# Performance work log

Measured on AMD Instinct MI355X. Metric: run time of the kernel, lower is better.

Reference implementation:

```python
import jax, jax.numpy as jnp
import numpy as np

EPS = 1e-5

def _layernorm(x, gamma, beta):
    # normalize over last (channel) axis, per point
    mu = jnp.mean(x, axis=-1, keepdims=True)
    var = jnp.mean(jnp.square(x - mu), axis=-1, keepdims=True)
    return (x - mu) * jax.lax.rsqrt(var + EPS) * gamma + beta

def setup_inputs() -> dict:
    key = jax.random.key(0)
    ks = jax.random.split(key, 12)
    B, N, C, F = 32, 4096, 3, 1024
    points = jax.random.normal(ks[0], (B, N, C), dtype=jnp.float32)
    mask = jax.random.randint(ks[1], (B, 1, N), 0, 2, dtype=jnp.int32)
    s = 0.05
    return {
        "points": points,
        "mask": mask,
        "w1": jax.random.normal(ks[2], (128, C), dtype=jnp.float32) * s,      # conv1 (no bias)
        "g1": jnp.ones((128,), jnp.float32),                                   # norm1 gamma
        "be1": jnp.zeros((128,), jnp.float32),                                 # norm1 beta
        "w2": jax.random.normal(ks[3], (256, 128), dtype=jnp.float32) * s,     # conv2
        "b2": jax.random.normal(ks[4], (256,), dtype=jnp.float32) * s,
        "w3": jax.random.normal(ks[5], (512, 512), dtype=jnp.float32) * s,     # conv3 (no bias)
        "g2": jnp.ones((512,), jnp.float32),                                   # norm2 gamma
        "be2": jnp.zeros((512,), jnp.float32),                                 # norm2 beta
        "w4": jax.random.normal(ks[6], (F, 512), dtype=jnp.float32) * s,       # conv4
        "b4": jax.random.normal(ks[7], (F,), dtype=jnp.float32) * s,
    }

def reference(points, mask, w1, g1, be1, w2, b2, w3, g2, be2, w4, b4):
    # points: [B, N, C]; mask: [B, 1, N]
    vis = (mask[:, 0, :] != 0).astype(points.dtype)[..., None]  # [B, N, 1]
    # conv1 (1x1, no bias) as point-wise matmul
    h0 = jnp.einsum('bnc,kc->bnk', points, w1)                  # [B, N, 128]
    # masked LayerNorm: LN is per-point over channels, so compute densely and zero invisible points
    h1 = _layernorm(h0, g1, be1) * vis
    h2 = jax.nn.relu(h1)
    h3 = jnp.einsum('bnk,ok->bno', h2, w2) + b2                 # [B, N, 256]
    gmax = jnp.max(h3, axis=1, keepdims=True)                   # [B, 1, 256]
    dist = jnp.concatenate([jnp.broadcast_to(gmax, h3.shape), h3], axis=-1)  # [B, N, 512]
    h4 = jnp.einsum('bno,po->bnp', dist, w3)                    # [B, N, 512]
    h5 = _layernorm(h4, g2, be2) * vis
    h6 = jax.nn.relu(h5)
    h7 = jnp.einsum('bnp,fp->bnf', h6, w4) + b4                 # [B, N, F]
    return jnp.max(h7, axis=1)                                  # [B, F]
```

## Files before the change

kernel.cpp:

```cpp
#include <hip/hip_runtime.h>
#include <stdint.h>

#define LN_EPS 1e-5f

static __device__ __forceinline__ unsigned short f2bf_bits(float f) {
  union { float f; unsigned u; } v; v.f = f;
  unsigned r = v.u + 0x7FFFu + ((v.u >> 16) & 1u);
  return (unsigned short)(r >> 16);
}
static __device__ __forceinline__ float bf2f(unsigned short h) {
  union { unsigned u; float f; } v; v.u = ((unsigned)h) << 16;
  return v.f;
}

typedef __bf16 bf16x8 __attribute__((ext_vector_type(8)));
typedef float floatx4 __attribute__((ext_vector_type(4)));

typedef __attribute__((address_space(1))) unsigned int* gas_ptr;
typedef __attribute__((address_space(3))) unsigned int* las_ptr;
static __device__ __forceinline__ void async_cp16(const void* g, void* l) {
  __builtin_amdgcn_global_load_lds((gas_ptr)g, (las_ptr)l, 16, 0, 0);
}

__global__ __launch_bounds__(256) void perm_kernel(
    const int* __restrict__ mask, int* __restrict__ newrow, int* __restrict__ cnt) {
  const int b = blockIdx.x, t = threadIdx.x;
  const int base = b * 4096 + t * 16;
  int v[16]; int s = 0;
#pragma unroll
  for (int i = 0; i < 16; ++i) { v[i] = (mask[base + i] != 0); s += v[i]; }
  const int lane = t & 63, wv = t >> 6;
  int scan = s;
  for (int o = 1; o < 64; o <<= 1) { int x = __shfl_up(scan, o); if (lane >= o) scan += x; }
  __shared__ int wsum[4], woff[4], stotal;
  if (lane == 63) wsum[wv] = scan;
  __syncthreads();
  if (t == 0) { int a = 0; for (int k = 0; k < 4; ++k) { woff[k] = a; a += wsum[k]; } stotal = a; cnt[b] = a; }
  __syncthreads();
  const int excl = scan - s + woff[wv];
  const int total = stotal;
  int run = 0;
#pragma unroll
  for (int i = 0; i < 16; ++i) {
    const int pos = t * 16 + i;
    const int visBefore = excl + run;
    newrow[b * 4096 + pos] = v[i] ? visBefore : total + (pos - visBefore);
    run += v[i];
  }
}

__global__ __launch_bounds__(256) void conv1_ln_kernel(
    const float* __restrict__ points,
    const float* __restrict__ w1, const float* __restrict__ g1,
    const float* __restrict__ be1, unsigned short* __restrict__ h2,
    const int* __restrict__ newrow, const int* __restrict__ cnt,
    const float* __restrict__ w2, const float* __restrict__ b2,
    const float* __restrict__ w3, const float* __restrict__ w4,
    unsigned short* __restrict__ w2b, unsigned short* __restrict__ w4b,
    unsigned short* __restrict__ w23b, float* __restrict__ vecb) {
  if (blockIdx.x >= 32768) {
    const int bb = blockIdx.x - 32768;
    if (bb < 2176) {
      int idx = bb * 256 + threadIdx.x;
      if (idx < 32768) w2b[idx] = f2bf_bits(w2[idx]);
      else w4b[idx - 32768] = f2bf_bits(w4[idx - 32768]);
    } else {
      const int tid = threadIdx.x;
      const int p = (bb - 2176) * 2 + (tid >> 7);
      const int c = tid & 127;
      const float* w3r = w3 + (size_t)p * 512 + 256;
      float s = 0.f;
      for (int k = 0; k < 256; ++k) s += w3r[k] * w2[k * 128 + c];
      w23b[p * 128 + c] = f2bf_bits(s);
      if (c == 0) {
        float vb = 0.f;
        for (int k = 0; k < 256; ++k) vb += w3r[k] * b2[k];
        vecb[p] = vb;
      }
    }
    return;
  }
  const int lane = threadIdx.x & 63;
  const int wv = threadIdx.x >> 6;
  const size_t p = (size_t)blockIdx.x * 4 + wv;
  const int dest = newrow[p];
  const int cntb = cnt[p >> 12];
  const int ceilv = (cntb + 127) & ~127;
  if (dest >= ceilv) return;
  const bool vis = (dest < cntb);
  const float x0 = points[p * 3 + 0];
  const float x1 = points[p * 3 + 1];
  const float x2 = points[p * 3 + 2];
  const int c0 = lane * 2, c1 = c0 + 1;
  float h00 = w1[c0 * 3] * x0 + w1[c0 * 3 + 1] * x1 + w1[c0 * 3 + 2] * x2;
  float h01 = w1[c1 * 3] * x0 + w1[c1 * 3 + 1] * x1 + w1[c1 * 3 + 2] * x2;
  float s = h00 + h01;
  for (int o = 32; o; o >>= 1) s += __shfl_xor(s, o);
  const float mu = s * (1.f / 128.f);
  const float d0 = h00 - mu, d1 = h01 - mu;
  float q = d0 * d0 + d1 * d1;
  for (int o = 32; o; o >>= 1) q += __shfl_xor(q, o);
  const float rs = rsqrtf(q * (1.f / 128.f) + LN_EPS);
  const float y0 = vis ? fmaxf(d0 * rs * g1[c0] + be1[c0], 0.f) : 0.f;
  const float y1 = vis ? fmaxf(d1 * rs * g1[c1] + be1[c1], 0.f) : 0.f;
  union { unsigned u; unsigned short s2[2]; } pk;
  pk.s2[0] = f2bf_bits(y0);
  pk.s2[1] = f2bf_bits(y1);
  const size_t prow = (p & ~(size_t)4095) + (size_t)dest;
  ((unsigned*)h2)[prow * 64 + lane] = pk.u;
}

__global__ __launch_bounds__(256) void gemm23_fused(
    const unsigned short* __restrict__ A,
    const unsigned short* __restrict__ w2b, const unsigned short* __restrict__ w23b,
    unsigned short* __restrict__ h46, float* __restrict__ pg,
    const float* __restrict__ b2, const float* __restrict__ vecb,
    const int* __restrict__ cnt, int M) {
  __shared__ __align__(16) char smA[2][128 * 64];
  __shared__ __align__(16) char smB[2][128 * 64];
  __shared__ float lmax[2][128];

  const int tid = threadIdx.x;
  const int lane = tid & 63;
  const int w = tid >> 6;
  const int wm = w >> 1, wn = w & 1;

  const int gid = blockIdx.x;
  const int xcd = gid & 7;
  const int slot = gid >> 3;
  const int rowsPerXcd = (M >> 7) >> 3;
  const int rowTile = xcd * rowsPerXcd + slot / 6;
  const int colTile = slot % 6;
  const bool isPG = (colTile < 2);
  const int colBase = isPG ? colTile * 128 : (colTile - 2) * 128;
  const size_t rowBase = (size_t)rowTile * 128;
  const unsigned short* Bw = isPG ? w2b : w23b;

  const int cntb = cnt[rowBase >> 12];
  const int rb = (int)(rowBase & 4095);
  if (rb >= cntb) {
    if (isPG) {
      if (tid < 128) pg[(size_t)rowTile * 256 + colBase + tid] = b2[colBase + tid];
    }
    return;
  }

  floatx4 acc[4][4];
  const floatx4 zero = {0.f, 0.f, 0.f, 0.f};
#pragma unroll
  for (int i = 0; i < 4; ++i)
#pragma unroll
    for (int j = 0; j < 4; ++j) acc[i][j] = zero;

  const int rSub = lane >> 2;
  const int cb16 = (lane & 3) * 16;
  const size_t Kb = 256;
  const char* gA = (const char*)A + (rowBase + (size_t)(w * 32 + rSub)) * Kb + cb16;
  const char* gB = (const char*)Bw + ((size_t)colBase + (size_t)(w * 32 + rSub)) * Kb + cb16;
  char* lA0 = smA[0] + w * 2048;
  char* lA1 = smA[1] + w * 2048;
  char* lB0 = smB[0] + w * 2048;
  char* lB1 = smB[1] + w * 2048;
  const size_t skip16 = 16 * Kb;

  const int fm = lane & 15, fq = lane >> 4;
  const int fOff = fm * 64 + fq * 16;
  const char* pa0 = smA[0] + wm * 64 * 64 + fOff;
  const char* pa1 = smA[1] + wm * 64 * 64 + fOff;
  const char* pb0 = smB[0] + wn * 64 * 64 + fOff;
  const char* pb1 = smB[1] + wn * 64 * 64 + fOff;

  for (int k0 = 0; k0 < 128; k0 += 64) {
    async_cp16(gA, lA0);
    async_cp16(gA + skip16, lA0 + 1024);
    async_cp16(gA + 64, lA1);
    async_cp16(gA + 64 + skip16, lA1 + 1024);
    async_cp16(gB, lB0);
    async_cp16(gB + skip16, lB0 + 1024);
    async_cp16(gB + 64, lB1);
    async_cp16(gB + 64 + skip16, lB1 + 1024);
    gA += 128; gB += 128;
    __syncthreads();
    bf16x8 af0[4], bg0[4], af1[4], bg1[4];
#pragma unroll
    for (int i = 0; i < 4; ++i) af0[i] = *(const bf16x8*)(pa0 + i * 16 * 64);
#pragma unroll
    for (int j = 0; j < 4; ++j) bg0[j] = *(const bf16x8*)(pb0 + j * 16 * 64);
#pragma unroll
    for (int i = 0; i < 4; ++i)
#pragma unroll
      for (int j = 0; j < 4; ++j)
        acc[i][j] = __builtin_amdgcn_mfma_f32_16x16x32_bf16(af0[i], bg0[j], acc[i][j], 0, 0, 0);
#pragma unroll
    for (int i = 0; i < 4; ++i) af1[i] = *(const bf16x8*)(pa1 + i * 16 * 64);
#pragma unroll
    for (int j = 0; j < 4; ++j) bg1[j] = *(const bf16x8*)(pb1 + j * 16 * 64);
#pragma unroll
    for (int i = 0; i < 4; ++i)
#pragma unroll
      for (int j = 0; j < 4; ++j)
        acc[i][j] = __builtin_amdgcn_mfma_f32_16x16x32_bf16(af1[i], bg1[j], acc[i][j], 0, 0, 0);
    __syncthreads();
  }

  if (isPG) {
    float m4[4] = {-1e30f, -1e30f, -1e30f, -1e30f};
#pragma unroll
    for (int j = 0; j < 4; ++j) {
      const float ex = b2[colBase + wn * 64 + j * 16 + fm];
#pragma unroll
      for (int i = 0; i < 4; ++i)
#pragma unroll
        for (int r = 0; r < 4; ++r) m4[j] = fmaxf(m4[j], acc[i][j][r] + ex);
      m4[j] = fmaxf(m4[j], __shfl_xor(m4[j], 16));
      m4[j] = fmaxf(m4[j], __shfl_xor(m4[j], 32));
    }
    const float sel = (fq == 0) ? m4[0] : (fq == 1) ? m4[1] : (fq == 2) ? m4[2] : m4[3];
    lmax[wm][wn * 64 + fq * 16 + fm] = sel;
    __syncthreads();
    if (tid < 128) {
      const float v = fmaxf(lmax[0][tid], lmax[1][tid]);
      pg[(size_t)rowTile * 256 + colBase + tid] = v;
    }
  } else {
#pragma unroll
    for (int j = 0; j < 4; ++j) {
      const int col = colBase + wn * 64 + j * 16 + fm;
      const float ex = vecb[col];
#pragma unroll
      for (int i = 0; i < 4; ++i) {
        const size_t row0 = rowBase + wm * 64 + i * 16 + fq * 4;
#pragma unroll
        for (int r = 0; r < 4; ++r) {
          h46[(row0 + r) * 512 + col] = f2bf_bits(acc[i][j][r] + ex);
        }
      }
    }
  }
}

template <int NCT>
__global__ __launch_bounds__(256) void gemm4_kernel(
    const unsigned short* __restrict__ A, const unsigned short* __restrict__ Bw,
    float* __restrict__ outp2, const int* __restrict__ cnt,
    int M, int N, int K) {
  __shared__ __align__(16) char smA[2][128 * 64];
  __shared__ __align__(16) char smB[2][128 * 64];
  __shared__ float lmax[2][128];

  const int tid = threadIdx.x;
  const int lane = tid & 63;
  const int w = tid >> 6;
  const int wm = w >> 1, wn = w & 1;

  const int gid = blockIdx.x;
  const int xcd = gid & 7;
  const int slot = gid >> 3;
  const int rowsPerXcd = (M >> 7) >> 3;
  const int rowTile = xcd * rowsPerXcd + slot / NCT;
  const int colTile = slot % NCT;
  const size_t rowBase = (size_t)rowTile * 128;
  const int colBase = colTile * 128;

  const int cntb = cnt[rowBase >> 12];
  const int rb = (int)(rowBase & 4095);
  if (rb >= cntb) {
    if (tid < 128) outp2[(size_t)rowTile * N + colBase + tid] = 0.f;
    return;
  }

  floatx4 acc[4][4];
  const floatx4 zero = {0.f, 0.f, 0.f, 0.f};
#pragma unroll
  for (int i = 0; i < 4; ++i)
#pragma unroll
    for (int j = 0; j < 4; ++j) acc[i][j] = zero;

  const int rSub = lane >> 2;
  const int cb16 = (lane & 3) * 16;
  const size_t Kb = (size_t)K * 2;
  const char* gA = (const char*)A + (rowBase + (size_t)(w * 32 + rSub)) * Kb + cb16;
  const char* gB = (const char*)Bw + ((size_t)colBase + (size_t)(w * 32 + rSub)) * Kb + cb16;
  char* lA0 = smA[0] + w * 2048;
  char* lA1 = smA[1] + w * 2048;
  char* lB0 = smB[0] + w * 2048;
  char* lB1 = smB[1] + w * 2048;
  const size_t skip16 = 16 * Kb;

  const int fm = lane & 15, fq = lane >> 4;
  const int fOff = fm * 64 + fq * 16;
  const char* pa0 = smA[0] + wm * 64 * 64 + fOff;
  const char* pa1 = smA[1] + wm * 64 * 64 + fOff;
  const char* pb0 = smB[0] + wn * 64 * 64 + fOff;
  const char* pb1 = smB[1] + wn * 64 * 64 + fOff;

  for (int k0 = 0; k0 < K; k0 += 64) {
    async_cp16(gA, lA0);
    async_cp16(gA + skip16, lA0 + 1024);
    async_cp16(gA + 64, lA1);
    async_cp16(gA + 64 + skip16, lA1 + 1024);
    async_cp16(gB, lB0);
    async_cp16(gB + skip16, lB0 + 1024);
    async_cp16(gB + 64, lB1);
    async_cp16(gB + 64 + skip16, lB1 + 1024);
    gA += 128; gB += 128;
    __syncthreads();
    bf16x8 af0[4], bg0[4], af1[4], bg1[4];
#pragma unroll
    for (int i = 0; i < 4; ++i) af0[i] = *(const bf16x8*)(pa0 + i * 16 * 64);
#pragma unroll
    for (int j = 0; j < 4; ++j) bg0[j] = *(const bf16x8*)(pb0 + j * 16 * 64);
#pragma unroll
    for (int i = 0; i < 4; ++i)
#pragma unroll
      for (int j = 0; j < 4; ++j)
        acc[i][j] = __builtin_amdgcn_mfma_f32_16x16x32_bf16(af0[i], bg0[j], acc[i][j], 0, 0, 0);
#pragma unroll
    for (int i = 0; i < 4; ++i) af1[i] = *(const bf16x8*)(pa1 + i * 16 * 64);
#pragma unroll
    for (int j = 0; j < 4; ++j) bg1[j] = *(const bf16x8*)(pb1 + j * 16 * 64);
#pragma unroll
    for (int i = 0; i < 4; ++i)
#pragma unroll
      for (int j = 0; j < 4; ++j)
        acc[i][j] = __builtin_amdgcn_mfma_f32_16x16x32_bf16(af1[i], bg1[j], acc[i][j], 0, 0, 0);
    __syncthreads();
  }

  float m4[4] = {-1e30f, -1e30f, -1e30f, -1e30f};
#pragma unroll
  for (int j = 0; j < 4; ++j) {
#pragma unroll
    for (int i = 0; i < 4; ++i)
#pragma unroll
      for (int r = 0; r < 4; ++r) m4[j] = fmaxf(m4[j], acc[i][j][r]);
    m4[j] = fmaxf(m4[j], __shfl_xor(m4[j], 16));
    m4[j] = fmaxf(m4[j], __shfl_xor(m4[j], 32));
  }
  const float sel = (fq == 0) ? m4[0] : (fq == 1) ? m4[1] : (fq == 2) ? m4[2] : m4[3];
  lmax[wm][wn * 64 + fq * 16 + fm] = sel;
  __syncthreads();
  if (tid < 128) {
    const float v = fmaxf(lmax[0][tid], lmax[1][tid]);
    outp2[(size_t)rowTile * N + colBase + tid] = v;
  }
}

__global__ __launch_bounds__(256) void gmax_cvec_kernel(
    const float* __restrict__ pg, const float* __restrict__ w3,
    float* __restrict__ cvec) {
  __shared__ float gm[256];
  const int b = blockIdx.x >> 2, quarter = blockIdx.x & 3;
  const int t = threadIdx.x;
  float m = -1e30f;
  for (int s = 0; s < 32; ++s) m = fmaxf(m, pg[((size_t)b * 32 + s) * 256 + t]);
  gm[t] = m;
  __syncthreads();
  const int lane = t & 63, wv = t >> 6;
  const float g0 = gm[lane * 4 + 0];
  const float g1 = gm[lane * 4 + 1];
  const float g2v = gm[lane * 4 + 2];
  const float g3 = gm[lane * 4 + 3];
  for (int pp = 0; pp < 32; ++pp) {
    const int p = quarter * 128 + wv * 32 + pp;
    const float4 wr = *(const float4*)(w3 + (size_t)p * 512 + lane * 4);
    float s = wr.x * g0 + wr.y * g1 + wr.z * g2v + wr.w * g3;
    for (int o = 32; o; o >>= 1) s += __shfl_xor(s, o);
    if (lane == 0) cvec[b * 512 + p] = s;
  }
}

__global__ __launch_bounds__(256) void ln2_kernel(
    unsigned short* __restrict__ h46, const int* __restrict__ cnt,
    const float* __restrict__ cvec,
    const float* __restrict__ g2, const float* __restrict__ be2) {
  const int lane = threadIdx.x & 63;
  const int wv = threadIdx.x >> 6;
  const size_t p = (size_t)blockIdx.x * 4 + wv;
  const int cb = cnt[p >> 12];
  const int pin = (int)(p & 4095);
  const int ceilv = (cb + 127) & ~127;
  if (pin >= ceilv) return;
  unsigned short* row = h46 + p * 512;
  const int c0 = lane * 8;
  if (pin >= cb) {
    const uint4 z = {0, 0, 0, 0};
    *(uint4*)(row + c0) = z;
    return;
  }
  const int b = (int)(p >> 12);
  union { uint4 v; unsigned short s[8]; } in;
  in.v = *(const uint4*)(row + c0);
  float cv[8];
  *(float4*)(cv) = *(const float4*)(cvec + b * 512 + c0);
  *(float4*)(cv + 4) = *(const float4*)(cvec + b * 512 + c0 + 4);
  float f[8];
  float s = 0.f;
#pragma unroll
  for (int k = 0; k < 8; ++k) { f[k] = bf2f(in.s[k]) + cv[k]; s += f[k]; }
  for (int o = 32; o; o >>= 1) s += __shfl_xor(s, o);
  const float mu = s * (1.f / 512.f);
  float q = 0.f;
#pragma unroll
  for (int k = 0; k < 8; ++k) { const float d = f[k] - mu; q += d * d; }
  for (int o = 32; o; o >>= 1) q += __shfl_xor(q, o);
  const float rs = rsqrtf(q * (1.f / 512.f) + LN_EPS);
  union { uint4 v; unsigned short s[8]; } outv;
#pragma unroll
  for (int k = 0; k < 8; ++k) {
    const float y = fmaxf((f[k] - mu) * rs * g2[c0 + k] + be2[c0 + k], 0.f);
    outv.s[k] = f2bf_bits(y);
  }
  *(uint4*)(row + c0) = outv.v;
}

__global__ __launch_bounds__(256) void final_kernel(
    const float* __restrict__ pmax, const float* __restrict__ b4,
    float* __restrict__ out) {
  const int idx = blockIdx.x * 256 + threadIdx.x;
  const int b = idx >> 10, f = idx & 1023;
  float m = -1e30f;
  for (int r = 0; r < 32; ++r) m = fmaxf(m, pmax[((size_t)(b * 32 + r)) * 1024 + f]);
  out[idx] = m + b4[f];
}

extern "C" void kernel_launch(void* const* d_in, const int* in_sizes, int n_in,
                              void* d_out, int out_size, void* d_ws, size_t ws_size,
                              hipStream_t stream) {
  const float* points = (const float*)d_in[0];
  const int* mask = (const int*)d_in[1];
  const float* w1 = (const float*)d_in[2];
  const float* g1 = (const float*)d_in[3];
  const float* be1 = (const float*)d_in[4];
  const float* w2 = (const float*)d_in[5];
  const float* b2 = (const float*)d_in[6];
  const float* w3 = (const float*)d_in[7];
  const float* g2 = (const float*)d_in[8];
  const float* be2 = (const float*)d_in[9];
  const float* w4 = (const float*)d_in[10];
  const float* b4 = (const float*)d_in[11];
  float* out = (float*)d_out;
  char* ws = (char*)d_ws;

  const size_t OFF_H46 = 0;
  const size_t OFF_H2 = 134217728;
  const size_t OFF_W2B = OFF_H2 + 33554432;
  const size_t OFF_W4B = OFF_W2B + 65536;
  const size_t OFF_W23B = OFF_W4B + 1048576;
  const size_t OFF_VECB = OFF_W23B + 131072;
  const size_t OFF_PG = OFF_VECB + 2048;
  const size_t OFF_CVEC = OFF_PG + 1048576;
  const size_t OFF_PMAX = OFF_CVEC + 65536;
  const size_t OFF_CNT = OFF_PMAX + 4194304;
  const size_t OFF_NEWROW = OFF_CNT + 4096;

  unsigned short* h2 = (unsigned short*)(ws + OFF_H2);
  unsigned short* h46 = (unsigned short*)(ws + OFF_H46);
  unsigned short* w2b = (unsigned short*)(ws + OFF_W2B);
  unsigned short* w4b = (unsigned short*)(ws + OFF_W4B);
  unsigned short* w23b = (unsigned short*)(ws + OFF_W23B);
  float* vecb = (float*)(ws + OFF_VECB);
  float* pg = (float*)(ws + OFF_PG);
  float* cvecp = (float*)(ws + OFF_CVEC);
  float* pmaxp = (float*)(ws + OFF_PMAX);
  int* cntp = (int*)(ws + OFF_CNT);
  int* newrow = (int*)(ws + OFF_NEWROW);

  perm_kernel<<<32, 256, 0, stream>>>(mask, newrow, cntp);
  conv1_ln_kernel<<<32768 + 2176 + 256, 256, 0, stream>>>(
      points, w1, g1, be1, h2, newrow, cntp, w2, b2, w3, w4, w2b, w4b, w23b, vecb);
  gemm23_fused<<<6144, 256, 0, stream>>>(h2, w2b, w23b, h46, pg, b2, vecb, cntp, 131072);
  gmax_cvec_kernel<<<128, 256, 0, stream>>>(pg, w3, cvecp);
  ln2_kernel<<<32768, 256, 0, stream>>>(h46, cntp, cvecp, g2, be2);
  gemm4_kernel<8><<<8192, 256, 0, stream>>>(h46, w4b, pmaxp, cntp, 131072, 1024, 512);
  final_kernel<<<128, 256, 0, stream>>>(pmaxp, b4, out);
}
```

Measured before the change: 276.6 us.

## Merge all stages into one cooperative persistent kernel with grid syncs

Replaces the seven separate kernel launches with a single cooperative mega-kernel. It runs a persistent grid sized from occupancy and separates the stages with grid.sync(). The aim is to remove per-launch overhead and the tail gaps between the small and large kernels. In exchange, blocks loop over virtual block IDs with occupancy capped at 3-4 blocks per CU, and tiles tied to the XCD mapping may lose locality. Each grid-wide barrier also has a cost, and the register pressure of the merged code may limit occupancy.

After: 651.0 us. 2.35x slower.

```diff
diff --git a/kernel.cpp b/kernel.cpp
--- a/kernel.cpp
+++ b/kernel.cpp
@@ -1,5 +1,8 @@
 #include <hip/hip_runtime.h>
+#include <hip/hip_cooperative_groups.h>
 #include <stdint.h>
+
+namespace cg = cooperative_groups;
 
 #define LN_EPS 1e-5f
 
@@ -22,406 +25,379 @@
   __builtin_amdgcn_global_load_lds((gas_ptr)g, (las_ptr)l, 16, 0, 0);
 }
 
-__global__ __launch_bounds__(256) void perm_kernel(
-    const int* __restrict__ mask, int* __restrict__ newrow, int* __restrict__ cnt) {
-  const int b = blockIdx.x, t = threadIdx.x;
-  const int base = b * 4096 + t * 16;
-  int v[16]; int s = 0;
-#pragma unroll
-  for (int i = 0; i < 16; ++i) { v[i] = (mask[base + i] != 0); s += v[i]; }
-  const int lane = t & 63, wv = t >> 6;
-  int scan = s;
-  for (int o = 1; o < 64; o <<= 1) { int x = __shfl_up(scan, o); if (lane >= o) scan += x; }
-  __shared__ int wsum[4], woff[4], stotal;
-  if (lane == 63) wsum[wv] = scan;
-  __syncthreads();
-  if (t == 0) { int a = 0; for (int k = 0; k < 4; ++k) { woff[k] = a; a += wsum[k]; } stotal = a; cnt[b] = a; }
-  __syncthreads();
-  const int excl = scan - s + woff[wv];
-  const int total = stotal;
-  int run = 0;
-#pragma unroll
-  for (int i = 0; i < 16; ++i) {
-    const int pos = t * 16 + i;
-    const int visBefore = excl + run;
-    newrow[b * 4096 + pos] = v[i] ? visBefore : total + (pos - visBefore);
-    run += v[i];
-  }
-}
-
-__global__ __launch_bounds__(256) void conv1_ln_kernel(
-    const float* __restrict__ points,
+__global__ __launch_bounds__(256, 3) void mega_kernel(
+    const float* __restrict__ points, const int* __restrict__ mask,
     const float* __restrict__ w1, const float* __restrict__ g1,
-    const float* __restrict__ be1, unsigned short* __restrict__ h2,
-    const int* __restrict__ newrow, const int* __restrict__ cnt,
-    const float* __restrict__ w2, const float* __restrict__ b2,
-    const float* __restrict__ w3, const float* __restrict__ w4,
+    const float* __restrict__ be1, const float* __restrict__ w2,
+    const float* __restrict__ b2, const float* __restrict__ w3,
+    const float* __restrict__ g2, const float* __restrict__ be2,
+    const float* __restrict__ w4, const float* __restrict__ b4,
+    float* __restrict__ out,
+    unsigned short* __restrict__ h2, unsigned short* __restrict__ h46,
     unsigned short* __restrict__ w2b, unsigned short* __restrict__ w4b,
-    unsigned short* __restrict__ w23b, float* __restrict__ vecb) {
-  if (blockIdx.x >= 32768) {
-    const int bb = blockIdx.x - 32768;
-    if (bb < 2176) {
-      int idx = bb * 256 + threadIdx.x;
-      if (idx < 32768) w2b[idx] = f2bf_bits(w2[idx]);
-      else w4b[idx - 32768] = f2bf_bits(w4[idx - 32768]);
-    } else {
-      const int tid = threadIdx.x;
-      const int p = (bb - 2176) * 2 + (tid >> 7);
-      const int c = tid & 127;
-      const float* w3r = w3 + (size_t)p * 512 + 256;
-      float s = 0.f;
-      for (int k = 0; k < 256; ++k) s += w3r[k] * w2[k * 128 + c];
-      w23b[p * 128 + c] = f2bf_bits(s);
-      if (c == 0) {
-        float vb = 0.f;
-        for (int k = 0; k < 256; ++k) vb += w3r[k] * b2[k];
-        vecb[p] = vb;
-      }
-    }
-    return;
-  }
-  const int lane = threadIdx.x & 63;
-  const int wv = threadIdx.x >> 6;
-  const size_t p = (size_t)blockIdx.x * 4 + wv;
-  const int dest = newrow[p];
-  const int cntb = cnt[p >> 12];
-  const int ceilv = (cntb + 127) & ~127;
-  if (dest >= ceilv) return;
-  const bool vis = (dest < cntb);
-  const float x0 = points[p * 3 + 0];
-  const float x1 = points[p * 3 + 1];
-  const float x2 = points[p * 3 + 2];
-  const int c0 = lane * 2, c1 = c0 + 1;
-  float h00 = w1[c0 * 3] * x0 + w1[c0 * 3 + 1] * x1 + w1[c0 * 3 + 2] * x2;
-  float h01 = w1[c1 * 3] * x0 + w1[c1 * 3 + 1] * x1 + w1[c1 * 3 + 2] * x2;
-  float s = h00 + h01;
-  for (int o = 32; o; o >>= 1) s += __shfl_xor(s, o);
-  const float mu = s * (1.f / 128.f);
-  const float d0 = h00 - mu, d1 = h01 - mu;
-  float q = d0 * d0 + d1 * d1;
-  for (int o = 32; o; o >>= 1) q += __shfl_xor(q, o);
-  const float rs = rsqrtf(q * (1.f / 128.f) + LN_EPS);
-  const float y0 = vis ? fmaxf(d0 * rs * g1[c0] + be1[c0], 0.f) : 0.f;
-  const float y1 = vis ? fmaxf(d1 * rs * g1[c1] + be1[c1], 0.f) : 0.f;
-  union { unsigned u; unsigned short s2[2]; } pk;
-  pk.s2[0] = f2bf_bits(y0);
-  pk.s2[1] = f2bf_bits(y1);
-  const size_t prow = (p & ~(size_t)4095) + (size_t)dest;
-  ((unsigned*)h2)[prow * 64 + lane] = pk.u;
-}
-
-__global__ __launch_bounds__(256) void gemm23_fused(
-    const unsigned short* __restrict__ A,
-    const unsigned short* __restrict__ w2b, const unsigned short* __restrict__ w23b,
-    unsigned short* __restrict__ h46, float* __restrict__ pg,
-    const float* __restrict__ b2, const float* __restrict__ vecb,
-    const int* __restrict__ cnt, int M) {
-  __shared__ __align__(16) char smA[2][128 * 64];
-  __shared__ __align__(16) char smB[2][128 * 64];
-  __shared__ float lmax[2][128];
-
+    unsigned short* __restrict__ w23b, float* __restrict__ vecb,
+    float* __restrict__ pg, float* __restrict__ cvec, float* __restrict__ pmax,
+    int* __restrict__ cnt, int* __restrict__ newrow) {
+  cg::grid_group grid = cg::this_grid();
+  __shared__ __align__(16) char SMEM[33792];
   const int tid = threadIdx.x;
   const int lane = tid & 63;
   const int w = tid >> 6;
+
+  for (int b = blockIdx.x; b < 32; b += gridDim.x) {
+    int* wsum = (int*)SMEM;
+    int* woff = ((int*)SMEM) + 4;
+    int* stot = ((int*)SMEM) + 8;
+    const int base = b * 4096 + tid * 16;
+    int v[16]; int s = 0;
+#pragma unroll
+    for (int i = 0; i < 16; ++i) { v[i] = (mask[base + i] != 0); s += v[i]; }
+    int scan = s;
+    for (int o = 1; o < 64; o <<= 1) { int x = __shfl_up(scan, o); if (lane >= o) scan += x; }
+    if (lane == 63) wsum[w] = scan;
+    __syncthreads();
+    if (tid == 0) {
+      int a = 0;
+      for (int k = 0; k < 4; ++k) { woff[k] = a; a += wsum[k]; }
+      stot[0] = a; cnt[b] = a;
+    }
+    __syncthreads();
+    const int excl = scan - s + woff[w];
+    const int total = stot[0];
+    int run = 0;
+#pragma unroll
+    for (int i = 0; i < 16; ++i) {
+      const int pos = tid * 16 + i;
+      const int visBefore = excl + run;
+      newrow[b * 4096 + pos] = v[i] ? visBefore : total + (pos - visBefore);
+      run += v[i];
+    }
+    __syncthreads();
+  }
+  grid.sync();
+
+  for (int vb = blockIdx.x; vb < 35200; vb += gridDim.x) {
+    if (vb >= 32768) {
+      const int bb = vb - 32768;
+      if (bb < 2176) {
+        int idx = bb * 256 + tid;
+        if (idx < 32768) w2b[idx] = f2bf_bits(w2[idx]);
+        else w4b[idx - 32768] = f2bf_bits(w4[idx - 32768]);
+      } else {
+        const int p = (bb - 2176) * 2 + (tid >> 7);
+        const int c = tid & 127;
+        const float* w3r = w3 + (size_t)p * 512 + 256;
+        float s = 0.f;
+        for (int k = 0; k < 256; ++k) s += w3r[k] * w2[k * 128 + c];
+        w23b[p * 128 + c] = f2bf_bits(s);
+        if (c == 0) {
+          float vbv = 0.f;
+          for (int k = 0; k < 256; ++k) vbv += w3r[k] * b2[k];
+          vecb[p] = vbv;
+        }
+      }
+    } else {
+      const size_t p = (size_t)vb * 4 + w;
+      const int dest = newrow[p];
+      const int cntb = cnt[p >> 12];
+      const int ceilv = (cntb + 127) & ~127;
+      if (dest < ceilv) {
+        const bool vis = (dest < cntb);
+        const float x0 = points[p * 3 + 0];
+        const float x1 = points[p * 3 + 1];
+        const float x2 = points[p * 3 + 2];
+        const int c0 = lane * 2, c1 = c0 + 1;
+        float h00 = w1[c0 * 3] * x0 + w1[c0 * 3 + 1] * x1 + w1[c0 * 3 + 2] * x2;
+        float h01 = w1[c1 * 3] * x0 + w1[c1 * 3 + 1] * x1 + w1[c1 * 3 + 2] * x2;
+        float s = h00 + h01;
+        for (int o = 32; o; o >>= 1) s += __shfl_xor(s, o);
+        const float mu = s * (1.f / 128.f);
+        const float d0 = h00 - mu, d1 = h01 - mu;
+        float q = d0 * d0 + d1 * d1;
+        for (int o = 32; o; o >>= 1) q += __shfl_xor(q, o);
+        const float rs = rsqrtf(q * (1.f / 128.f) + LN_EPS);
+        const float y0 = vis ? fmaxf(d0 * rs * g1[c0] + be1[c0], 0.f) : 0.f;
+        const float y1 = vis ? fmaxf(d1 * rs * g1[c1] + be1[c1], 0.f) : 0.f;
+        union { unsigned u; unsigned short s2[2]; } pk;
+        pk.s2[0] = f2bf_bits(y0);
+        pk.s2[1] = f2bf_bits(y1);
+        const size_t prow = (p & ~(size_t)4095) + (size_t)dest;
+        ((unsigned*)h2)[prow * 64 + lane] = pk.u;
+      }
+    }
+  }
+  grid.sync();
+
+  char* smA0 = SMEM;
+  char* smA1 = SMEM + 8192;
+  char* smB0 = SMEM + 16384;
+  char* smB1 = SMEM + 24576;
+  float* lmax = (float*)(SMEM + 32768);
   const int wm = w >> 1, wn = w & 1;
-
-  const int gid = blockIdx.x;
-  const int xcd = gid & 7;
-  const int slot = gid >> 3;
-  const int rowsPerXcd = (M >> 7) >> 3;
-  const int rowTile = xcd * rowsPerXcd + slot / 6;
-  const int colTile = slot % 6;
-  const bool isPG = (colTile < 2);
-  const int colBase = isPG ? colTile * 128 : (colTile - 2) * 128;
-  const size_t rowBase = (size_t)rowTile * 128;
-  const unsigned short* Bw = isPG ? w2b : w23b;
-
-  const int cntb = cnt[rowBase >> 12];
-  const int rb = (int)(rowBase & 4095);
-  if (rb >= cntb) {
-    if (isPG) {
-      if (tid < 128) pg[(size_t)rowTile * 256 + colBase + tid] = b2[colBase + tid];
-    }
-    return;
-  }
-
-  floatx4 acc[4][4];
-  const floatx4 zero = {0.f, 0.f, 0.f, 0.f};
-#pragma unroll
-  for (int i = 0; i < 4; ++i)
-#pragma unroll
-    for (int j = 0; j < 4; ++j) acc[i][j] = zero;
-
+  const int fm = lane & 15, fq = lane >> 4;
   const int rSub = lane >> 2;
   const int cb16 = (lane & 3) * 16;
-  const size_t Kb = 256;
-  const char* gA = (const char*)A + (rowBase + (size_t)(w * 32 + rSub)) * Kb + cb16;
-  const char* gB = (const char*)Bw + ((size_t)colBase + (size_t)(w * 32 + rSub)) * Kb + cb16;
-  char* lA0 = smA[0] + w * 2048;
-  char* lA1 = smA[1] + w * 2048;
-  char* lB0 = smB[0] + w * 2048;
-  char* lB1 = smB[1] + w * 2048;
-  const size_t skip16 = 16 * Kb;
-
-  const int fm = lane & 15, fq = lane >> 4;
   const int fOff = fm * 64 + fq * 16;
-  const char* pa0 = smA[0] + wm * 64 * 64 + fOff;
-  const char* pa1 = smA[1] + wm * 64 * 64 + fOff;
-  const char* pb0 = smB[0] + wn * 64 * 64 + fOff;
-  const char* pb1 = smB[1] + wn * 64 * 64 + fOff;
-
-  for (int k0 = 0; k0 < 128; k0 += 64) {
-    async_cp16(gA, lA0);
-    async_cp16(gA + skip16, lA0 + 1024);
-    async_cp16(gA + 64, lA1);
-    async_cp16(gA + 64 + skip16, lA1 + 1024);
-    async_cp16(gB, lB0);
-    async_cp16(gB + skip16, lB0 + 1024);
-    async_cp16(gB + 64, lB1);
-    async_cp16(gB + 64 + skip16, lB1 + 1024);
-    gA += 128; gB += 128;
+
+  for (int gid = blockIdx.x; gid < 6144; gid += gridDim.x) {
+    const int xcd = gid & 7;
+    const int slot = gid >> 3;
+    const int rowTile = xcd * 128 + slot / 6;
+    const int colTile = slot % 6;
+    const bool isPG = (colTile < 2);
+    const int colBase = isPG ? colTile * 128 : (colTile - 2) * 128;
+    const size_t rowBase = (size_t)rowTile * 128;
+    const unsigned short* Bw = isPG ? w2b : w23b;
+    const int cntb = cnt[rowBase >> 12];
+    const int rb = (int)(rowBase & 4095);
+    if (rb >= cntb) {
+      if (isPG && tid < 128) pg[(size_t)rowTile * 256 + colBase + tid] = b2[colBase + tid];
+      continue;
+    }
+    floatx4 acc[4][4];
+    const floatx4 zero = {0.f, 0.f, 0.f, 0.f};
+#pragma unroll
+    for (int i = 0; i < 4; ++i)
+#pragma unroll
+      for (int j = 0; j < 4; ++j) acc[i][j] = zero;
+
+    const size_t Kb = 256;
+    const char* gA = (const char*)h2 + (rowBase + (size_t)(w * 32 + rSub)) * Kb + cb16;
+    const char* gB = (const char*)Bw + ((size_t)colBase + (size_t)(w * 32 + rSub)) * Kb + cb16;
+    const size_t skip16 = 16 * Kb;
+    char* lA0 = smA0 + w * 2048;
+    char* lA1 = smA1 + w * 2048;
+    char* lB0 = smB0 + w * 2048;
+    char* lB1 = smB1 + w * 2048;
+    const char* pa0 = smA0 + wm * 64 * 64 + fOff;
+    const char* pa1 = smA1 + wm * 64 * 64 + fOff;
+    const char* pb0 = smB0 + wn * 64 * 64 + fOff;
+    const char* pb1 = smB1 + wn * 64 * 64 + fOff;
+
+    for (int k0 = 0; k0 < 128; k0 += 64) {
+      async_cp16(gA, lA0);
+      async_cp16(gA + skip16, lA0 + 1024);
+      async_cp16(gA + 64, lA1);
+      async_cp16(gA + 64 + skip16, lA1 + 1024);
+      async_cp16(gB, lB0);
+      async_cp16(gB + skip16, lB0 + 1024);
+      async_cp16(gB + 64, lB1);
+      async_cp16(gB + 64 + skip16, lB1 + 1024);
+      gA += 128; gB += 128;
+      __syncthreads();
+      bf16x8 af0[4], bg0[4], af1[4], bg1[4];
+#pragma unroll
+      for (int i = 0; i < 4; ++i) af0[i] = *(const bf16x8*)(pa0 + i * 16 * 64);
+#pragma unroll
+      for (int j = 0; j < 4; ++j) bg0[j] = *(const bf16x8*)(pb0 + j * 16 * 64);
+#pragma unroll
+      for (int i = 0; i < 4; ++i)
+#pragma unroll
+        for (int j = 0; j < 4; ++j)
+          acc[i][j] = __builtin_amdgcn_mfma_f32_16x16x32_bf16(af0[i], bg0[j], acc[i][j], 0, 0, 0);
+#pragma unroll
+      for (int i = 0; i < 4; ++i) af1[i] = *(const bf16x8*)(pa1 + i * 16 * 64);
+#pragma unroll
+      for (int j = 0; j < 4; ++j) bg1[j] = *(const bf16x8*)(pb1 + j * 16 * 64);
+#pragma unroll
+      for (int i = 0; i < 4; ++i)
+#pragma unroll
+        for (int j = 0; j < 4; ++j)
+          acc[i][j] = __builtin_amdgcn_mfma_f32_16x16x32_bf16(af1[i], bg1[j], acc[i][j], 0, 0, 0);
+      __syncthreads();
+    }
+
+    if (isPG) {
+      float m4[4] = {-1e30f, -1e30f, -1e30f, -1e30f};
+#pragma unroll
+      for (int j = 0; j < 4; ++j) {
+        const float ex = b2[colBase + wn * 64 + j * 16 + fm];
+#pragma unroll
+        for (int i = 0; i < 4; ++i)
+#pragma unroll
+          for (int r = 0; r < 4; ++r) m4[j] = fmaxf(m4[j], acc[i][j][r] + ex);
+        m4[j] = fmaxf(m4[j], __shfl_xor(m4[j], 16));
+        m4[j] = fmaxf(m4[j], __shfl_xor(m4[j], 32));
+      }
+      const float sel = (fq == 0) ? m4[0] : (fq == 1) ? m4[1] : (fq == 2) ? m4[2] : m4[3];
+      lmax[wm * 128 + wn * 64 + fq * 16 + fm] = sel;
+      __syncthreads();
+      if (tid < 128) {
+        const float v = fmaxf(lmax[tid], lmax[128 + tid]);
+        pg[(size_t)rowTile * 256 + colBase + tid] = v;
+      }
+    } else {
+#pragma unroll
+      for (int j = 0; j < 4; ++j) {
+        const int col = colBase + wn * 64 + j * 16 + fm;
+        const float ex = vecb[col];
+#pragma unroll
+        for (int i = 0; i < 4; ++i) {
+          const size_t row0 = rowBase + wm * 64 + i * 16 + fq * 4;
+#pragma unroll
+          for (int r = 0; r < 4; ++r) {
+            h46[(row0 + r) * 512 + col] = f2bf_bits(acc[i][j][r] + ex);
+          }
+        }
+      }
+    }
+  }
+  grid.sync();
+
+  if (blockIdx.x < 128) {
+    float* gm = (float*)SMEM;
+    const int b = blockIdx.x >> 2, quarter = blockIdx.x & 3;
+    float m = -1e30f;
+    for (int s = 0; s < 32; ++s) m = fmaxf(m, pg[((size_t)b * 32 + s) * 256 + tid]);
+    gm[tid] = m;
     __syncthreads();
-    bf16x8 af0[4], bg0[4], af1[4], bg1[4];
-#pragma unroll
-    for (int i = 0; i < 4; ++i) af0[i] = *(const bf16x8*)(pa0 + i * 16 * 64);
-#pragma unroll
-    for (int j = 0; j < 4; ++j) bg0[j] = *(const bf16x8*)(pb0 + j * 16 * 64);
+    const float g0 = gm[lane * 4 + 0];
+    const float g1v = gm[lane * 4 + 1];
+    const float g2v = gm[lane * 4 + 2];
+    const float g3 = gm[lane * 4 + 3];
+    for (int pp = 0; pp < 32; ++pp) {
+      const int p = quarter * 128 + w * 32 + pp;
+      const float4 wr = *(const float4*)(w3 + (size_t)p * 512 + lane * 4);
+      float s = wr.x * g0 + wr.y * g1v + wr.z * g2v + wr.w * g3;
+      for (int o = 32; o; o >>= 1) s += __shfl_xor(s, o);
+      if (lane == 0) cvec[b * 512 + p] = s;
+    }
+  }
+  grid.sync();
+
+  for (int vb = blockIdx.x; vb < 32768; vb += gridDim.x) {
+    const size_t p = (size_t)vb * 4 + w;
+    const int cb = cnt[p >> 12];
+    const int pin = (int)(p & 4095);
+    const int ceilv = (cb + 127) & ~127;
+    if (pin >= ceilv) continue;
+    unsigned short* row = h46 + p * 512;
+    const int c0 = lane * 8;
+    if (pin >= cb) {
+      const uint4 z = {0, 0, 0, 0};
+      *(uint4*)(row + c0) = z;
+      continue;
+    }
+    const int b = (int)(p >> 12);
+    union { uint4 v; unsigned short s[8]; } in;
+    in.v = *(const uint4*)(row + c0);
+    float cv[8];
+    *(float4*)(cv) = *(const float4*)(cvec + b * 512 + c0);
+    *(float4*)(cv + 4) = *(const float4*)(cvec + b * 512 + c0 + 4);
+    float f[8];
+    float s = 0.f;
+#pragma unroll
+    for (int k = 0; k < 8; ++k) { f[k] = bf2f(in.s[k]) + cv[k]; s += f[k]; }
+    for (int o = 32; o; o >>= 1) s += __shfl_xor(s, o);
+    const float mu = s * (1.f / 512.f);
+    float q = 0.f;
+#pragma unroll
+    for (int k = 0; k < 8; ++k) { const float d = f[k] - mu; q += d * d; }
+    for (int o = 32; o; o >>= 1) q += __shfl_xor(q, o);
+    const float rs = rsqrtf(q * (1.f / 512.f) + LN_EPS);
+    union { uint4 v; unsigned short s[8]; } outv;
+#pragma unroll
+    for (int k = 0; k < 8; ++k) {
+      const float y = fmaxf((f[k] - mu) * rs * g2[c0 + k] + be2[c0 + k], 0.f);
+      outv.s[k] = f2bf_bits(y);
+    }
+    *(uint4*)(row + c0) = outv.v;
+  }
+  grid.sync();
+
+  for (int gid = blockIdx.x; gid < 8192; gid += gridDim.x) {
+    const int xcd = gid & 7;
+    const int slot = gid >> 3;
+    const int rowTile = xcd * 128 + slot / 8;
+    const int colTile = slot % 8;
+    const size_t rowBase = (size_t)rowTile * 128;
+    const int colBase = colTile * 128;
+    const int cntb = cnt[rowBase >> 12];
+    const int rb = (int)(rowBase & 4095);
+    if (rb >= cntb) {
+      if (tid < 128) pmax[(size_t)rowTile * 1024 + colBase + tid] = 0.f;
+      continue;
+    }
+    floatx4 acc[4][4];
+    const floatx4 zero = {0.f, 0.f, 0.f, 0.f};
 #pragma unroll
     for (int i = 0; i < 4; ++i)
 #pragma unroll
-      for (int j = 0; j < 4; ++j)
-        acc[i][j] = __builtin_amdgcn_mfma_f32_16x16x32_bf16(af0[i], bg0[j], acc[i][j], 0, 0, 0);
-#pragma unroll
-    for (int i = 0; i < 4; ++i) af1[i] = *(const bf16x8*)(pa1 + i * 16 * 64);
-#pragma unroll
-    for (int j = 0; j < 4; ++j) bg1[j] = *(const bf16x8*)(pb1 + j * 16 * 64);
-#pragma unroll
-    for (int i = 0; i < 4; ++i)
-#pragma unroll
-      for (int j = 0; j < 4; ++j)
-        acc[i][j] = __builtin_amdgcn_mfma_f32_16x16x32_bf16(af1[i], bg1[j], acc[i][j], 0, 0, 0);
-    __syncthreads();
-  }
-
-  if (isPG) {
+      for (int j = 0; j < 4; ++j) acc[i][j] = zero;
+
+    const size_t Kb = 1024;
+    const char* gA = (const char*)h46 + (rowBase + (size_t)(w * 32 + rSub)) * Kb + cb16;
+    const char* gB = (const char*)w4b + ((size_t)colBase + (size_t)(w * 32 + rSub)) * Kb + cb16;
+    const size_t skip16 = 16 * Kb;
+    char* lA0 = smA0 + w * 2048;
+    char* lA1 = smA1 + w * 2048;
+    char* lB0 = smB0 + w * 2048;
+    char* lB1 = smB1 + w * 2048;
+    const char* pa0 = smA0 + wm * 64 * 64 + fOff;
+    const char* pa1 = smA1 + wm * 64 * 64 + fOff;
+    const char* pb0 = smB0 + wn * 64 * 64 + fOff;
+    const char* pb1 = smB1 + wn * 64 * 64 + fOff;
+
+    for (int k0 = 0; k0 < 512; k0 += 64) {
+      async_cp16(gA, lA0);
+      async_cp16(gA + skip16, lA0 + 1024);
+      async_cp16(gA + 64, lA1);
+      async_cp16(gA + 64 + skip16, lA1 + 1024);
+      async_cp16(gB, lB0);
+      async_cp16(gB + skip16, lB0 + 1024);
+      async_cp16(gB + 64, lB1);
+      async_cp16(gB + 64 + skip16, lB1 + 1024);
+      gA += 128; gB += 128;
+      __syncthreads();
+      bf16x8 af0[4], bg0[4], af1[4], bg1[4];
+#pragma unroll
+      for (int i = 0; i < 4; ++i) af0[i] = *(const bf16x8*)(pa0 + i * 16 * 64);
+#pragma unroll
+      for (int j = 0; j < 4; ++j) bg0[j] = *(const bf16x8*)(pb0 + j * 16 * 64);
+#pragma unroll
+      for (int i = 0; i < 4; ++i)
+#pragma unroll
+        for (int j = 0; j < 4; ++j)
+          acc[i][j] = __builtin_amdgcn_mfma_f32_16x16x32_bf16(af0[i], bg0[j], acc[i][j], 0, 0, 0);
+#pragma unroll
+      for (int i = 0; i < 4; ++i) af1[i] = *(const bf16x8*)(pa1 + i * 16 * 64);
+#pragma unroll
+      for (int j = 0; j < 4; ++j) bg1[j] = *(const bf16x8*)(pb1 + j * 16 * 64);
+#pragma unroll
+      for (int i = 0; i < 4; ++i)
+#pragma unroll
+        for (int j = 0; j < 4; ++j)
+          acc[i][j] = __builtin_amdgcn_mfma_f32_16x16x32_bf16(af1[i], bg1[j], acc[i][j], 0, 0, 0);
+      __syncthreads();
+    }
+
     float m4[4] = {-1e30f, -1e30f, -1e30f, -1e30f};
 #pragma unroll
     for (int j = 0; j < 4; ++j) {
-      const float ex = b2[colBase + wn * 64 + j * 16 + fm];
 #pragma unroll
       for (int i = 0; i < 4; ++i)
 #pragma unroll
-        for (int r = 0; r < 4; ++r) m4[j] = fmaxf(m4[j], acc[i][j][r] + ex);
+        for (int r = 0; r < 4; ++r) m4[j] = fmaxf(m4[j], acc[i][j][r]);
       m4[j] = fmaxf(m4[j], __shfl_xor(m4[j], 16));
       m4[j] = fmaxf(m4[j], __shfl_xor(m4[j], 32));
     }
     const float sel = (fq == 0) ? m4[0] : (fq == 1) ? m4[1] : (fq == 2) ? m4[2] : m4[3];
-    lmax[wm][wn * 64 + fq * 16 + fm] = sel;
+    lmax[wm * 128 + wn * 64 + fq * 16 + fm] = sel;
     __syncthreads();
     if (tid < 128) {
-      const float v = fmaxf(lmax[0][tid], lmax[1][tid]);
-      pg[(size_t)rowTile * 256 + colBase + tid] = v;
-    }
-  } else {
-#pragma unroll
-    for (int j = 0; j < 4; ++j) {
-      const int col = colBase + wn * 64 + j * 16 + fm;
-      const float ex = vecb[col];
-#pragma unroll
-      for (int i = 0; i < 4; ++i) {
-        const size_t row0 = rowBase + wm * 64 + i * 16 + fq * 4;
-#pragma unroll
-        for (int r = 0; r < 4; ++r) {
-          h46[(row0 + r) * 512 + col] = f2bf_bits(acc[i][j][r] + ex);
-        }
-      }
-    }
-  }
-}
-
-template <int NCT>
-__global__ __launch_bounds__(256) void gemm4_kernel(
-    const unsigned short* __restrict__ A, const unsigned short* __restrict__ Bw,
-    float* __restrict__ outp2, const int* __restrict__ cnt,
-    int M, int N, int K) {
-  __shared__ __align__(16) char smA[2][128 * 64];
-  __shared__ __align__(16) char smB[2][128 * 64];
-  __shared__ float lmax[2][128];
-
-  const int tid = threadIdx.x;
-  const int lane = tid & 63;
-  const int w = tid >> 6;
-  const int wm = w >> 1, wn = w & 1;
-
-  const int gid = blockIdx.x;
-  const int xcd = gid & 7;
-  const int slot = gid >> 3;
-  const int rowsPerXcd = (M >> 7) >> 3;
-  const int rowTile = xcd * rowsPerXcd + slot / NCT;
-  const int colTile = slot % NCT;
-  const size_t rowBase = (size_t)rowTile * 128;
-  const int colBase = colTile * 128;
-
-  const int cntb = cnt[rowBase >> 12];
-  const int rb = (int)(rowBase & 4095);
-  if (rb >= cntb) {
-    if (tid < 128) outp2[(size_t)rowTile * N + colBase + tid] = 0.f;
-    return;
-  }
-
-  floatx4 acc[4][4];
-  const floatx4 zero = {0.f, 0.f, 0.f, 0.f};
-#pragma unroll
-  for (int i = 0; i < 4; ++i)
-#pragma unroll
-    for (int j = 0; j < 4; ++j) acc[i][j] = zero;
-
-  const int rSub = lane >> 2;
-  const int cb16 = (lane & 3) * 16;
-  const size_t Kb = (size_t)K * 2;
-  const char* gA = (const char*)A + (rowBase + (size_t)(w * 32 + rSub)) * Kb + cb16;
-  const char* gB = (const char*)Bw + ((size_t)colBase + (size_t)(w * 32 + rSub)) * Kb + cb16;
-  char* lA0 = smA[0] + w * 2048;
-  char* lA1 = smA[1] + w * 2048;
-  char* lB0 = smB[0] + w * 2048;
-  char* lB1 = smB[1] + w * 2048;
-  const size_t skip16 = 16 * Kb;
-
-  const int fm = lane & 15, fq = lane >> 4;
-  const int fOff = fm * 64 + fq * 16;
-  const char* pa0 = smA[0] + wm * 64 * 64 + fOff;
-  const char* pa1 = smA[1] + wm * 64 * 64 + fOff;
-  const char* pb0 = smB[0] + wn * 64 * 64 + fOff;
-  const char* pb1 = smB[1] + wn * 64 * 64 + fOff;
-
-  for (int k0 = 0; k0 < K; k0 += 64) {
-    async_cp16(gA, lA0);
-    async_cp16(gA + skip16, lA0 + 1024);
-    async_cp16(gA + 64, lA1);
-    async_cp16(gA + 64 + skip16, lA1 + 1024);
-    async_cp16(gB, lB0);
-    async_cp16(gB + skip16, lB0 + 1024);
-    async_cp16(gB + 64, lB1);
-    async_cp16(gB + 64 + skip16, lB1 + 1024);
-    gA += 128; gB += 128;
-    __syncthreads();
-    bf16x8 af0[4], bg0[4], af1[4], bg1[4];
-#pragma unroll
-    for (int i = 0; i < 4; ++i) af0[i] = *(const bf16x8*)(pa0 + i * 16 * 64);
-#pragma unroll
-    for (int j = 0; j < 4; ++j) bg0[j] = *(const bf16x8*)(pb0 + j * 16 * 64);
-#pragma unroll
-    for (int i = 0; i < 4; ++i)
-#pragma unroll
-      for (int j = 0; j < 4; ++j)
-        acc[i][j] = __builtin_amdgcn_mfma_f32_16x16x32_bf16(af0[i], bg0[j], acc[i][j], 0, 0, 0);
-#pragma unroll
-    for (int i = 0; i < 4; ++i) af1[i] = *(const bf16x8*)(pa1 + i * 16 * 64);
-#pragma unroll
-    for (int j = 0; j < 4; ++j) bg1[j] = *(const bf16x8*)(pb1 + j * 16 * 64);
-#pragma unroll
-    for (int i = 0; i < 4; ++i)
-#pragma unroll
-      for (int j = 0; j < 4; ++j)
-        acc[i][j] = __builtin_amdgcn_mfma_f32_16x16x32_bf16(af1[i], bg1[j], acc[i][j], 0, 0, 0);
-    __syncthreads();
-  }
-
-  float m4[4] = {-1e30f, -1e30f, -1e30f, -1e30f};
-#pragma unroll
-  for (int j = 0; j < 4; ++j) {
-#pragma unroll
-    for (int i = 0; i < 4; ++i)
-#pragma unroll
-      for (int r = 0; r < 4; ++r) m4[j] = fmaxf(m4[j], acc[i][j][r]);
-    m4[j] = fmaxf(m4[j], __shfl_xor(m4[j], 16));
-    m4[j] = fmaxf(m4[j], __shfl_xor(m4[j], 32));
-  }
-  const float sel = (fq == 0) ? m4[0] : (fq == 1) ? m4[1] : (fq == 2) ? m4[2] : m4[3];
-  lmax[wm][wn * 64 + fq * 16 + fm] = sel;
-  __syncthreads();
-  if (tid < 128) {
-    const float v = fmaxf(lmax[0][tid], lmax[1][tid]);
-    outp2[(size_t)rowTile * N + colBase + tid] = v;
-  }
-}
-
-__global__ __launch_bounds__(256) void gmax_cvec_kernel(
-    const float* __restrict__ pg, const float* __restrict__ w3,
-    float* __restrict__ cvec) {
-  __shared__ float gm[256];
-  const int b = blockIdx.x >> 2, quarter = blockIdx.x & 3;
-  const int t = threadIdx.x;
-  float m = -1e30f;
-  for (int s = 0; s < 32; ++s) m = fmaxf(m, pg[((size_t)b * 32 + s) * 256 + t]);
-  gm[t] = m;
-  __syncthreads();
-  const int lane = t & 63, wv = t >> 6;
-  const float g0 = gm[lane * 4 + 0];
-  const float g1 = gm[lane * 4 + 1];
-  const float g2v = gm[lane * 4 + 2];
-  const float g3 = gm[lane * 4 + 3];
-  for (int pp = 0; pp < 32; ++pp) {
-    const int p = quarter * 128 + wv * 32 + pp;
-    const float4 wr = *(const float4*)(w3 + (size_t)p * 512 + lane * 4);
-    float s = wr.x * g0 + wr.y * g1 + wr.z * g2v + wr.w * g3;
-    for (int o = 32; o; o >>= 1) s += __shfl_xor(s, o);
-    if (lane == 0) cvec[b * 512 + p] = s;
-  }
-}
-
-__global__ __launch_bounds__(256) void ln2_kernel(
-    unsigned short* __restrict__ h46, const int* __restrict__ cnt,
-    const float* __restrict__ cvec,
-    const float* __restrict__ g2, const float* __restrict__ be2) {
-  const int lane = threadIdx.x & 63;
-  const int wv = threadIdx.x >> 6;
-  const size_t p = (size_t)blockIdx.x * 4 + wv;
-  const int cb = cnt[p >> 12];
-  const int pin = (int)(p & 4095);
-  const int ceilv = (cb + 127) & ~127;
-  if (pin >= ceilv) return;
-  unsigned short* row = h46 + p * 512;
-  const int c0 = lane * 8;
-  if (pin >= cb) {
-    const uint4 z = {0, 0, 0, 0};
-    *(uint4*)(row + c0) = z;
-    return;
-  }
-  const int b = (int)(p >> 12);
-  union { uint4 v; unsigned short s[8]; } in;
-  in.v = *(const uint4*)(row + c0);
-  float cv[8];
-  *(float4*)(cv) = *(const float4*)(cvec + b * 512 + c0);
-  *(float4*)(cv + 4) = *(const float4*)(cvec + b * 512 + c0 + 4);
-  float f[8];
-  float s = 0.f;
-#pragma unroll
-  for (int k = 0; k < 8; ++k) { f[k] = bf2f(in.s[k]) + cv[k]; s += f[k]; }
-  for (int o = 32; o; o >>= 1) s += __shfl_xor(s, o);
-  const float mu = s * (1.f / 512.f);
-  float q = 0.f;
-#pragma unroll
-  for (int k = 0; k < 8; ++k) { const float d = f[k] - mu; q += d * d; }
-  for (int o = 32; o; o >>= 1) q += __shfl_xor(q, o);
-  const float rs = rsqrtf(q * (1.f / 512.f) + LN_EPS);
-  union { uint4 v; unsigned short s[8]; } outv;
-#pragma unroll
-  for (int k = 0; k < 8; ++k) {
-    const float y = fmaxf((f[k] - mu) * rs * g2[c0 + k] + be2[c0 + k], 0.f);
-    outv.s[k] = f2bf_bits(y);
-  }
-  *(uint4*)(row + c0) = outv.v;
-}
-
-__global__ __launch_bounds__(256) void final_kernel(
-    const float* __restrict__ pmax, const float* __restrict__ b4,
-    float* __restrict__ out) {
-  const int idx = blockIdx.x * 256 + threadIdx.x;
-  const int b = idx >> 10, f = idx & 1023;
-  float m = -1e30f;
-  for (int r = 0; r < 32; ++r) m = fmaxf(m, pmax[((size_t)(b * 32 + r)) * 1024 + f]);
-  out[idx] = m + b4[f];
+      const float v = fmaxf(lmax[tid], lmax[128 + tid]);
+      pmax[(size_t)rowTile * 1024 + colBase + tid] = v;
+    }
+  }
+  grid.sync();
+
+  for (int vb = blockIdx.x; vb < 128; vb += gridDim.x) {
+    const int idx = vb * 256 + tid;
+    const int b = idx >> 10, f = idx & 1023;
+    float m = -1e30f;
+    for (int r = 0; r < 32; ++r) m = fmaxf(m, pmax[((size_t)(b * 32 + r)) * 1024 + f]);
+    out[idx] = m + b4[f];
+  }
 }
 
 extern "C" void kernel_launch(void* const* d_in, const int* in_sizes, int n_in,
@@ -466,12 +442,18 @@
   int* cntp = (int*)(ws + OFF_CNT);
   int* newrow = (int*)(ws + OFF_NEWROW);
 
-  perm_kernel<<<32, 256, 0, stream>>>(mask, newrow, cntp);
-  conv1_ln_kernel<<<32768 + 2176 + 256, 256, 0, stream>>>(
-      points, w1, g1, be1, h2, newrow, cntp, w2, b2, w3, w4, w2b, w4b, w23b, vecb);
-  gemm23_fused<<<6144, 256, 0, stream>>>(h2, w2b, w23b, h46, pg, b2, vecb, cntp, 131072);
-  gmax_cvec_kernel<<<128, 256, 0, stream>>>(pg, w3, cvecp);
-  ln2_kernel<<<32768, 256, 0, stream>>>(h46, cntp, cvecp, g2, be2);
-  gemm4_kernel<8><<<8192, 256, 0, stream>>>(h46, w4b, pmaxp, cntp, 131072, 1024, 512);
-  final_kernel<<<128, 256, 0, stream>>>(pmaxp, b4, out);
+  int maxB = 0;
+  hipOccupancyMaxActiveBlocksPerMultiprocessor(&maxB, mega_kernel, 256, 0);
+  if (maxB < 1) maxB = 1;
+  if (maxB > 4) maxB = 4;
+  int grid = maxB * 256;
+
+  void* args[] = {
+    (void*)&points, (void*)&mask, (void*)&w1, (void*)&g1, (void*)&be1,
+    (void*)&w2, (void*)&b2, (void*)&w3, (void*)&g2, (void*)&be2,
+    (void*)&w4, (void*)&b4, (void*)&out,
+    (void*)&h2, (void*)&h46, (void*)&w2b, (void*)&w4b, (void*)&w23b, (void*)&vecb,
+    (void*)&pg, (void*)&cvecp, (void*)&pmaxp, (void*)&cntp, (void*)&newrow
+  };
+  hipLaunchCooperativeKernel((void*)mega_kernel, dim3(grid), dim3(256), args, 0, stream);
 }
```
